# Performance work log

Measured on AMD Instinct MI355X. Metric: run time of the kernel, lower is better.

## Reference

```python
import jax, jax.numpy as jnp
import numpy as np

MAX_DIM = 1024
VOCAB = 257
DEPTH = 6
Q_DIM = MAX_DIM // 4  # 256
EXP_DIMS = [1, 2, 4, 8, 16, 32, 64, 128]  # expander sizes: current_q doubles up to Q_DIM
BATCH, SEQ = 8, 4096


def qlinear(q, W):
    """Quaternion Hamilton-product linear.
    q: [..., in, 4] (last dim = r,i,j,k components), W: [4, out, in] (stacked r,i,j,k weights).
    Returns [..., out, 4].
    """
    # P[..., o, w, a] = F.linear(component_a, W_w)  -> all 16 small GEMMs in one einsum
    P = jnp.einsum('...ia,woi->...owa', q, W)
    Pr, Pi, Pj, Pk = P[..., 0, :], P[..., 1, :], P[..., 2, :], P[..., 3, :]  # each [..., out, 4]
    out_r = Pr[..., 0] - Pi[..., 1] - Pj[..., 2] - Pk[..., 3]
    out_i = Pi[..., 0] + Pr[..., 1] + Pk[..., 2] - Pj[..., 3]
    out_j = Pj[..., 0] - Pk[..., 1] + Pr[..., 2] + Pi[..., 3]
    out_k = Pk[..., 0] + Pj[..., 1] - Pi[..., 2] + Pr[..., 3]
    return jnp.stack([out_r, out_i, out_j, out_k], axis=-1)


def qnormalize(q):
    norm = jnp.linalg.norm(q, axis=-1, keepdims=True)
    return q / (norm + 1e-8)


def setup_inputs() -> dict:
    key = jax.random.key(0)
    ks = jax.random.split(key, 4 + len(EXP_DIMS))
    inp = {}
    inp['x'] = jax.random.randint(ks[0], (BATCH, SEQ), 0, VOCAB)
    inp['emb'] = jax.random.normal(ks[1], (VOCAB, 4), dtype=jnp.float32)
    for idx, cq in enumerate(EXP_DIMS):
        scale = cq ** (-0.5)
        inp[f'w_exp{idx}'] = jax.random.uniform(ks[2 + idx], (4, cq, cq), jnp.float32, -scale, scale)
    scale = Q_DIM ** (-0.5)
    inp['w_layers'] = jax.random.uniform(ks[-2], (DEPTH, 4, Q_DIM, Q_DIM), jnp.float32, -scale, scale)
    inp['w_head'] = jax.random.normal(ks[-1], (VOCAB, MAX_DIM), dtype=jnp.float32) * MAX_DIM ** (-0.5)
    return inp


def reference(x, emb, w_exp0, w_exp1, w_exp2, w_exp3, w_exp4, w_exp5, w_exp6, w_exp7,
              w_layers, w_head):
    q = emb[x][:, :, None, :]  # [B, S, 1, 4]
    for w in (w_exp0, w_exp1, w_exp2, w_exp3, w_exp4, w_exp5, w_exp6, w_exp7):
        delta = jnp.tanh(qlinear(q, w))
        q = jnp.concatenate([q + delta, q - delta], axis=2)  # doubles quaternion dim
    for d in range(DEPTH):
        q = qnormalize(qlinear(q, w_layers[d]))
    stability_loss = jnp.mean(jnp.abs(q[..., 0]))
    h_flat = q.reshape(x.shape[0], x.shape[1], -1)  # [B, S, MAX_DIM]
    logits = jnp.einsum('bsd,vd->bsv', h_flat, w_head)
    return (logits, stability_loss)
```

## Files before the change

kernel.cpp:

```cpp
#include <hip/hip_runtime.h>


typedef _Float16 f16x8 __attribute__((ext_vector_type(8)));
typedef float    f32x4 __attribute__((ext_vector_type(4)));

#define GL2LDS16(gp, lp) __builtin_amdgcn_global_load_lds(                     \
    (const __attribute__((address_space(1))) void*)(gp),                       \
    (__attribute__((address_space(3))) void*)(lp), 16, 0, 0)

__device__ __forceinline__ unsigned short f2h(float f) {
  union { _Float16 h; unsigned short u; } c;
  c.h = (_Float16)f;
  return c.u;
}
__device__ __forceinline__ float h2f(unsigned short u) {
  union { unsigned short u; _Float16 h; } c;
  c.u = u;
  return (float)c.h;
}

__global__ __launch_bounds__(256) void expand_ham(
    const float* __restrict__ w, unsigned short* __restrict__ out,
    int cq, int kbits, int total) {
  int id = blockIdx.x * 256 + threadIdx.x;
  if (id >= total) return;
  const int K = 1 << kbits;
  const int n = id >> kbits;
  const int k = id & (K - 1);
  float val = 0.f;
  if (n < 4 * cq) {
    const int o = n >> 2, a = n & 3, i = k >> 2, b = k & 3;
    const int   comp[4][4] = {{0,1,2,3},{1,0,3,2},{2,3,0,1},{3,2,1,0}};
    const float sgn [4][4] = {{1.f,-1.f,-1.f,-1.f},{1.f,1.f,1.f,-1.f},
                              {1.f,-1.f,1.f,1.f},{1.f,1.f,-1.f,1.f}};
    val = sgn[a][b] * w[comp[a][b] * cq * cq + o * cq + i];
  }
  out[id] = f2h(val);
}

__global__ __launch_bounds__(256) void expand_ham6(
    const float* __restrict__ w, unsigned short* __restrict__ out) {
  const int id = blockIdx.x * 256 + threadIdx.x;
  const int d = id >> 20;
  const int r = id & 1048575;
  const int n = r >> 10, k = r & 1023;
  const int o = n >> 2, a = n & 3, i = k >> 2, b = k & 3;
  const int   comp[4][4] = {{0,1,2,3},{1,0,3,2},{2,3,0,1},{3,2,1,0}};
  const float sgn [4][4] = {{1.f,-1.f,-1.f,-1.f},{1.f,1.f,1.f,-1.f},
                            {1.f,-1.f,1.f,1.f},{1.f,1.f,-1.f,1.f}};
  const float val =
      sgn[a][b] * w[d * 262144 + comp[a][b] * 65536 + o * 256 + i];
  out[id] = f2h(val);
}

__global__ __launch_bounds__(256) void conv_head(
    const float* __restrict__ wh, unsigned short* __restrict__ out) {
  int id = blockIdx.x * 256 + threadIdx.x;
  int v = id >> 10, k = id & 1023;
  out[id] = f2h(v < 257 ? wh[v * 1024 + k] : 0.f);
}

template <int CQ>
__device__ __forceinline__ void exp_step(float (&q)[16][4],
                                         const float* __restrict__ w) {
  float d[CQ][4];
#pragma unroll
  for (int o = 0; o < CQ; o++) {
    float pr = 0.f, pi = 0.f, pj = 0.f, pk = 0.f;
#pragma unroll
    for (int i = 0; i < CQ; i++) {
      const float wr = w[0 * CQ * CQ + o * CQ + i];
      const float wi = w[1 * CQ * CQ + o * CQ + i];
      const float wj = w[2 * CQ * CQ + o * CQ + i];
      const float wk = w[3 * CQ * CQ + o * CQ + i];
      const float qr = q[i][0], qi = q[i][1], qj = q[i][2], qk = q[i][3];
      pr += wr * qr - wi * qi - wj * qj - wk * qk;
      pi += wi * qr + wr * qi + wk * qj - wj * qk;
      pj += wj * qr - wk * qi + wr * qj + wi * qk;
      pk += wk * qr + wj * qi - wi * qj + wr * qk;
    }
    d[o][0] = tanhf(pr); d[o][1] = tanhf(pi);
    d[o][2] = tanhf(pj); d[o][3] = tanhf(pk);
  }
#pragma unroll
  for (int o = 0; o < CQ; o++)
#pragma unroll
    for (int a = 0; a < 4; a++) {
      const float dd = d[o][a], qq = q[o][a];
      q[o][a]      = qq + dd;
      q[CQ + o][a] = qq - dd;
    }
}

__global__ __launch_bounds__(256) void embed_expand(
    const int* __restrict__ x, const float* __restrict__ emb,
    const float* __restrict__ w0, const float* __restrict__ w1,
    const float* __restrict__ w2, const float* __restrict__ w3,
    unsigned short* __restrict__ out) {
  const int t = blockIdx.x * 256 + threadIdx.x;
  float q[16][4];
  const int v = x[t];
  const float4 e = *(const float4*)(emb + v * 4);
  q[0][0] = e.x; q[0][1] = e.y; q[0][2] = e.z; q[0][3] = e.w;
  exp_step<1>(q, w0);
  exp_step<2>(q, w1);
  exp_step<4>(q, w2);
  exp_step<8>(q, w3);
  ushort4* o4 = (ushort4*)(out + (size_t)t * 64);
#pragma unroll
  for (int c = 0; c < 16; c++) {
    ushort4 u;
    u.x = f2h(q[c][0]); u.y = f2h(q[c][1]);
    u.z = f2h(q[c][2]); u.w = f2h(q[c][3]);
    o4[c] = u;
  }
}

template <int EPI>
__global__ __launch_bounds__(256) void gemm_epi(
    const unsigned short* __restrict__ W,
    const unsigned short* __restrict__ Act,
    unsigned short* __restrict__ OutB, float* __restrict__ OutF,
    int K, int Nreal, int ldout) {
  __shared__ unsigned short WtL[128 * 32];
  __shared__ unsigned short WtH[128 * 32];
  __shared__ unsigned short AtL[128 * 32];
  __shared__ unsigned short AtH[128 * 32];

  const int tid  = threadIdx.x;
  const int wave = tid >> 6;
  const int lane = tid & 63;
  const int l15  = lane & 15;
  const int quad = lane >> 4;

  const int Gx = gridDim.x;
  const int L  = blockIdx.y * Gx + blockIdx.x;
  const int j  = L & 7;
  const int s  = L >> 3;
  const int nblock = (s % Gx) * 128;
  const int mblock = (32 * j + s / Gx) * 128;
  const int wn = (wave & 1) * 64;
  const int wm = (wave >> 1) * 64;

  f32x4 acc[4][4];
  const f32x4 zero = {0.f, 0.f, 0.f, 0.f};
#pragma unroll
  for (int a = 0; a < 4; a++)
#pragma unroll
    for (int b = 0; b < 4; b++) acc[a][b] = zero;

  const int row0 = tid >> 2;
  const int sub  = tid & 3;
  const unsigned short* gW0 = W   + (size_t)(nblock + row0)      * K + sub * 8;
  const unsigned short* gW1 = W   + (size_t)(nblock + row0 + 64) * K + sub * 8;
  const unsigned short* gA0 = Act + (size_t)(mblock + row0)      * K + sub * 8;
  const unsigned short* gA1 = Act + (size_t)(mblock + row0 + 64) * K + sub * 8;
  unsigned short* lWL0 = &WtL[wave * 512];
  unsigned short* lWL1 = &WtL[2048 + wave * 512];
  unsigned short* lWH0 = &WtH[wave * 512];
  unsigned short* lWH1 = &WtH[2048 + wave * 512];
  unsigned short* lAL0 = &AtL[wave * 512];
  unsigned short* lAL1 = &AtL[2048 + wave * 512];
  unsigned short* lAH0 = &AtH[wave * 512];
  unsigned short* lAH1 = &AtH[2048 + wave * 512];

  for (int kb = 0; kb < K; kb += 64) {
    GL2LDS16(gW0 + kb,      lWL0);
    GL2LDS16(gW1 + kb,      lWL1);
    GL2LDS16(gW0 + kb + 32, lWH0);
    GL2LDS16(gW1 + kb + 32, lWH1);
    GL2LDS16(gA0 + kb,      lAL0);
    GL2LDS16(gA1 + kb,      lAL1);
    GL2LDS16(gA0 + kb + 32, lAH0);
    GL2LDS16(gA1 + kb + 32, lAH1);
    __syncthreads();

    {
      f16x8 afr[4], bfr[4];
#pragma unroll
      for (int tn = 0; tn < 4; tn++)
        afr[tn] = *(const f16x8*)&WtL[(wn + tn * 16 + l15) * 32 + quad * 8];
#pragma unroll
      for (int tm = 0; tm < 4; tm++)
        bfr[tm] = *(const f16x8*)&AtL[(wm + tm * 16 + l15) * 32 + quad * 8];
#pragma unroll
      for (int tn = 0; tn < 4; tn++)
#pragma unroll
        for (int tm = 0; tm < 4; tm++)
          acc[tn][tm] = __builtin_amdgcn_mfma_f32_16x16x32_f16(
              afr[tn], bfr[tm], acc[tn][tm], 0, 0, 0);
    }
    {
      f16x8 afr[4], bfr[4];
#pragma unroll
      for (int tn = 0; tn < 4; tn++)
        afr[tn] = *(const f16x8*)&WtH[(wn + tn * 16 + l15) * 32 + quad * 8];
#pragma unroll
      for (int tm = 0; tm < 4; tm++)
        bfr[tm] = *(const f16x8*)&AtH[(wm + tm * 16 + l15) * 32 + quad * 8];
#pragma unroll
      for (int tn = 0; tn < 4; tn++)
#pragma unroll
        for (int tm = 0; tm < 4; tm++)
          acc[tn][tm] = __builtin_amdgcn_mfma_f32_16x16x32_f16(
              afr[tn], bfr[tm], acc[tn][tm], 0, 0, 0);
    }
    __syncthreads();
  }

#pragma unroll
  for (int tn = 0; tn < 4; tn++) {
    const int n = nblock + wn + tn * 16 + quad * 4;
    if (n < Nreal) {
#pragma unroll
      for (int tm = 0; tm < 4; tm++) {
        const int token = mblock + wm + tm * 16 + l15;
        const f32x4 v = acc[tn][tm];
        const unsigned short* ip = Act + (size_t)token * K + n;
        const float i0 = h2f(ip[0]), i1 = h2f(ip[1]);
        const float i2 = h2f(ip[2]), i3 = h2f(ip[3]);
        const float d0 = tanhf(v[0]), d1 = tanhf(v[1]);
        const float d2 = tanhf(v[2]), d3 = tanhf(v[3]);
        ushort4 up, um;
        up.x = f2h(i0 + d0); up.y = f2h(i1 + d1);
        up.z = f2h(i2 + d2); up.w = f2h(i3 + d3);
        um.x = f2h(i0 - d0); um.y = f2h(i1 - d1);
        um.z = f2h(i2 - d2); um.w = f2h(i3 - d3);
        *(ushort4*)&OutB[(size_t)token * ldout + n] = up;
        *(ushort4*)&OutB[(size_t)token * ldout + Nreal + n] = um;
      }
    }
  }
}

template <int EPI>
__global__ __launch_bounds__(256, 4) void gemm8p(
    const unsigned short* __restrict__ W,
    const unsigned short* __restrict__ Act,
    unsigned short* __restrict__ OutB, float* __restrict__ OutF,
    int K, int NW, int ldout) {
  __shared__ unsigned short S[2 * 8192];
  __shared__ float lsum[4];

  const int tid  = threadIdx.x;
  const int wave = tid >> 6;
  const int lane = tid & 63;
  const int l15  = lane & 15;
  const int quad = lane >> 4;
  const int wr   = wave >> 1;
  const int wc   = wave & 1;

  const int Gx = gridDim.x;
  const int L  = blockIdx.y * Gx + blockIdx.x;
  const int j  = L & 7;
  const int s  = L >> 3;
  const int mblock = (j * (gridDim.y >> 3) + s / Gx) * 128;
  const int nblock = (s % Gx) * 128;
  const int NT = K >> 5;

  f32x4 acc[4][4];
  const f32x4 zero = {0.f, 0.f, 0.f, 0.f};
#pragma unroll
  for (int a = 0; a < 4; a++)
#pragma unroll
    for (int b = 0; b < 4; b++) acc[a][b] = zero;

  const int rw = tid >> 2;
  const int sl = (tid & 3) ^ ((tid >> 3) & 3);
  const int wrow0 = nblock + rw;
  const int wrow1 = nblock + 64 + rw;
  const int cw0 = wrow0 < NW ? wrow0 : NW - 1;
  const int cw1 = wrow1 < NW ? wrow1 : NW - 1;
  const unsigned short* sW0 = W   + (size_t)cw0 * K + sl * 8;
  const unsigned short* sW1 = W   + (size_t)cw1 * K + sl * 8;
  const unsigned short* sB0 = Act + (size_t)(mblock + rw)      * K + sl * 8;
  const unsigned short* sB1 = Act + (size_t)(mblock + 64 + rw) * K + sl * 8;

  const int swz = (quad * 8) ^ ((l15 & 6) << 2);

  {
    unsigned short* d0 = S + tid * 8;
    GL2LDS16(sW0, d0);
    GL2LDS16(sW1, d0 + 2048);
    GL2LDS16(sB0, d0 + 4096);
    GL2LDS16(sB1, d0 + 6144);
    if (NT > 1) {
      unsigned short* d1 = S + 8192 + tid * 8;
      GL2LDS16(sW0 + 32, d1);
      GL2LDS16(sW1 + 32, d1 + 2048);
      GL2LDS16(sB0 + 32, d1 + 4096);
      GL2LDS16(sB1 + 32, d1 + 6144);
      asm volatile("s_waitcnt vmcnt(4)" ::: "memory");
    } else {
      asm volatile("s_waitcnt vmcnt(0)" ::: "memory");
    }
  }
  __builtin_amdgcn_s_barrier();
  __builtin_amdgcn_sched_barrier(0);

#pragma unroll 2
  for (int kt = 0; kt < NT; ++kt) {
    const unsigned short* SA = S + (kt & 1) * 8192;
    const unsigned short* SB = SA + 4096;

    f16x8 af[4], bf[4];
#pragma unroll
    for (int t4 = 0; t4 < 4; t4++)
      af[t4] = *(const f16x8*)(SA + (wr * 64 + t4 * 16 + l15) * 32 + swz);
#pragma unroll
    for (int t4 = 0; t4 < 4; t4++)
      bf[t4] = *(const f16x8*)(SB + (wc * 64 + t4 * 16 + l15) * 32 + swz);

    asm volatile("s_waitcnt lgkmcnt(0)" ::: "memory");
    __builtin_amdgcn_s_barrier();
    __builtin_amdgcn_sched_barrier(0);
    if (kt + 2 < NT) {
      const int kb = (kt + 2) * 32;
      unsigned short* d = S + (kt & 1) * 8192 + tid * 8;
      GL2LDS16(sW0 + kb, d);
      GL2LDS16(sW1 + kb, d + 2048);
      GL2LDS16(sB0 + kb, d + 4096);
      GL2LDS16(sB1 + kb, d + 6144);
    }

    __builtin_amdgcn_s_setprio(1);
#pragma unroll
    for (int tn = 0; tn < 4; tn++)
#pragma unroll
      for (int tm = 0; tm < 4; tm++)
        acc[tn][tm] = __builtin_amdgcn_mfma_f32_16x16x32_f16(
            af[tn], bf[tm], acc[tn][tm], 0, 0, 0);
    __builtin_amdgcn_s_setprio(0);

    if (kt < NT - 1) {
      if (kt + 2 < NT) asm volatile("s_waitcnt vmcnt(4)" ::: "memory");
      else             asm volatile("s_waitcnt vmcnt(0)" ::: "memory");
      __builtin_amdgcn_s_barrier();
      __builtin_amdgcn_sched_barrier(0);
    }
  }

  if constexpr (EPI == 0) {
#pragma unroll
    for (int tn = 0; tn < 4; tn++) {
      const int n = nblock + wr * 64 + tn * 16 + quad * 4;
#pragma unroll
      for (int tm = 0; tm < 4; tm++) {
        const int token = mblock + wc * 64 + tm * 16 + l15;
        const f32x4 v = acc[tn][tm];
        const unsigned short* ip = Act + (size_t)token * K + n;
        const float i0 = h2f(ip[0]), i1 = h2f(ip[1]);
        const float i2 = h2f(ip[2]), i3 = h2f(ip[3]);
        const float d0 = tanhf(v[0]), d1 = tanhf(v[1]);
        const float d2 = tanhf(v[2]), d3 = tanhf(v[3]);
        ushort4 up, um;
        up.x = f2h(i0 + d0); up.y = f2h(i1 + d1);
        up.z = f2h(i2 + d2); up.w = f2h(i3 + d3);
        um.x = f2h(i0 - d0); um.y = f2h(i1 - d1);
        um.z = f2h(i2 - d2); um.w = f2h(i3 - d3);
        *(ushort4*)&OutB[(size_t)token * ldout + n] = up;
        *(ushort4*)&OutB[(size_t)token * ldout + NW + n] = um;
      }
    }
  } else if constexpr (EPI == 1 || EPI == 2) {
    float loss = 0.f;
#pragma unroll
    for (int tn = 0; tn < 4; tn++) {
      const int n = nblock + wr * 64 + tn * 16 + quad * 4;
#pragma unroll
      for (int tm = 0; tm < 4; tm++) {
        const int token = mblock + wc * 64 + tm * 16 + l15;
        const f32x4 v = acc[tn][tm];
        const float nrm =
            sqrtf(v[0] * v[0] + v[1] * v[1] + v[2] * v[2] + v[3] * v[3]);
        const float inv = 1.f / (nrm + 1e-8f);
        ushort4 u;
        u.x = f2h(v[0] * inv); u.y = f2h(v[1] * inv);
        u.z = f2h(v[2] * inv); u.w = f2h(v[3] * inv);
        *(ushort4*)&OutB[(size_t)token * 1024 + n] = u;
        if constexpr (EPI == 2) loss += fabsf(v[0] * inv);
      }
    }
    if constexpr (EPI == 2) {
#pragma unroll
      for (int off = 32; off > 0; off >>= 1) loss += __shfl_down(loss, off);
      if (lane == 0) lsum[wave] = loss;
      __syncthreads();
      if (tid == 0) {
        float t = lsum[0] + lsum[1] + lsum[2] + lsum[3];
        atomicAdd(OutF, t * (1.f / 8388608.f));
      }
    }
  } else {
#pragma unroll
    for (int tn = 0; tn < 4; tn++) {
      const int n = nblock + wr * 64 + tn * 16 + quad * 4;
      if (n < 257) {
#pragma unroll
        for (int tm = 0; tm < 4; tm++) {
          const int token = mblock + wc * 64 + tm * 16 + l15;
          const f32x4 v = acc[tn][tm];
#pragma unroll
          for (int r = 0; r < 4; r++)
            if (n + r < 257) OutF[(size_t)token * 257 + n + r] = v[r];
        }
      }
    }
  }
}

extern "C" void kernel_launch(void* const* d_in, const int* in_sizes, int n_in,
                              void* d_out, int out_size, void* d_ws,
                              size_t ws_size, hipStream_t stream) {
  const int*   x    = (const int*)d_in[0];
  const float* emb  = (const float*)d_in[1];
  const float* we0  = (const float*)d_in[2];
  const float* we1  = (const float*)d_in[3];
  const float* we2  = (const float*)d_in[4];
  const float* we3  = (const float*)d_in[5];
  const float* we4  = (const float*)d_in[6];
  const float* we5  = (const float*)d_in[7];
  const float* we6  = (const float*)d_in[8];
  const float* we7  = (const float*)d_in[9];
  const float* wlay = (const float*)d_in[10];
  const float* wh   = (const float*)d_in[11];
  float* out = (float*)d_out;

  char* p = (char*)d_ws;
  auto alloc = [&](size_t bytes) {
    void* r = (void*)p;
    p += (bytes + 255) & ~(size_t)255;
    return r;
  };
  unsigned short* act0 = (unsigned short*)alloc(32768ull * 1024 * 2);
  unsigned short* act1 = (unsigned short*)alloc(32768ull * 1024 * 2);
  unsigned short* E4 = (unsigned short*)alloc(128 * 64 * 2);
  unsigned short* E5 = (unsigned short*)alloc(128 * 128 * 2);
  unsigned short* E6 = (unsigned short*)alloc(256 * 256 * 2);
  unsigned short* E7 = (unsigned short*)alloc(512 * 512 * 2);
  unsigned short* EL = (unsigned short*)alloc(6ull * 1024 * 1024 * 2);
  unsigned short* WH = (unsigned short*)alloc(384 * 1024 * 2);

  hipMemsetAsync(out + 8421376, 0, 4, stream);

  expand_ham<<<dim3(8192 / 256), 256, 0, stream>>>(we4, E4, 16, 6, 128 * 64);
  expand_ham<<<dim3(16384 / 256), 256, 0, stream>>>(we5, E5, 32, 7, 128 * 128);
  expand_ham<<<dim3(65536 / 256), 256, 0, stream>>>(we6, E6, 64, 8, 256 * 256);
  expand_ham<<<dim3(262144 / 256), 256, 0, stream>>>(we7, E7, 128, 9,
                                                     512 * 512);
  expand_ham6<<<dim3(6 * 1048576 / 256), 256, 0, stream>>>(wlay, EL);
  conv_head<<<dim3(384 * 1024 / 256), 256, 0, stream>>>(wh, WH);

  embed_expand<<<dim3(128), 256, 0, stream>>>(x, emb, we0, we1, we2, we3, act0);

  gemm_epi<0><<<dim3(1, 256), 256, 0, stream>>>(E4, act0, act1, nullptr, 64,
                                                64, 128);
  gemm_epi<0><<<dim3(1, 256), 256, 0, stream>>>(E5, act1, act0, nullptr, 128,
                                                128, 256);
  gemm8p<0><<<dim3(2, 256), 256, 0, stream>>>(E6, act0, act1, nullptr, 256,
                                              256, 512);
  gemm8p<0><<<dim3(4, 256), 256, 0, stream>>>(E7, act1, act0, nullptr, 512,
                                              512, 1024);

  unsigned short* a = act0;
  unsigned short* b = act1;
  for (int d = 0; d < 5; d++) {
    gemm8p<1><<<dim3(8, 256), 256, 0, stream>>>(EL + (size_t)d * 1048576, a, b,
                                                nullptr, 1024, 1024, 1024);
    unsigned short* t = a; a = b; b = t;
  }
  gemm8p<2><<<dim3(8, 256), 256, 0, stream>>>(EL + 5ull * 1048576, a, b,
                                              out + 8421376, 1024, 1024, 1024);
  { unsigned short* t = a; a = b; b = t; }

  gemm8p<3><<<dim3(3, 256), 256, 0, stream>>>(WH, a, nullptr, out, 1024, 384,
                                              0);
}
```

Before: 973.9 us.

## Load activation operand directly into registers and retile GEMM to 64x256 blocks

Replaces the 128x128 LDS-staged GEMM with a 64(N)x256(M) tile. Each wave loads its own 64 activation rows straight from global memory into registers with inline-asm dwordx4 loads, and only the weight tile is staged through LDS in a 4-deep ring buffer. This cuts LDS traffic and LDS reads for the activation operand and shrinks shared memory per block. The costs are higher register pressure (launch bounds drop to 3 blocks per CU), uncoalesced row-strided global loads, and no W row clamping for the head GEMM. The head weights are padded to 384 rows, so that case stays in bounds.

```diff
diff --git a/kernel.cpp b/kernel.cpp
--- a/kernel.cpp
+++ b/kernel.cpp
@@ -7,6 +7,10 @@
 #define GL2LDS16(gp, lp) __builtin_amdgcn_global_load_lds(                     \
     (const __attribute__((address_space(1))) void*)(gp),                       \
     (__attribute__((address_space(3))) void*)(lp), 16, 0, 0)
+
+#define BLOAD(dst, voff, imm)                                                  \
+  asm volatile("global_load_dwordx4 %0, %1, %2 offset:" #imm                   \
+               : "=v"(dst) : "v"(voff), "s"(bbase))
 
 __device__ __forceinline__ unsigned short f2h(float f) {
   union { _Float16 h; unsigned short u; } c;
@@ -234,12 +238,12 @@
 }
 
 template <int EPI>
-__global__ __launch_bounds__(256, 4) void gemm8p(
+__global__ __launch_bounds__(256, 3) void gemm_bg(
     const unsigned short* __restrict__ W,
     const unsigned short* __restrict__ Act,
     unsigned short* __restrict__ OutB, float* __restrict__ OutF,
     int K, int NW, int ldout) {
-  __shared__ unsigned short S[2 * 8192];
+  __shared__ unsigned short S[4 * 2048];
   __shared__ float lsum[4];
 
   const int tid  = threadIdx.x;
@@ -247,15 +251,13 @@
   const int lane = tid & 63;
   const int l15  = lane & 15;
   const int quad = lane >> 4;
-  const int wr   = wave >> 1;
-  const int wc   = wave & 1;
 
   const int Gx = gridDim.x;
   const int L  = blockIdx.y * Gx + blockIdx.x;
   const int j  = L & 7;
   const int s  = L >> 3;
-  const int mblock = (j * (gridDim.y >> 3) + s / Gx) * 128;
-  const int nblock = (s % Gx) * 128;
+  const int mblock = (j * (gridDim.y >> 3) + s / Gx) * 256;
+  const int nblock = (s % Gx) * 64;
   const int NT = K >> 5;
 
   f32x4 acc[4][4];
@@ -265,88 +267,117 @@
 #pragma unroll
     for (int b = 0; b < 4; b++) acc[a][b] = zero;
 
-  const int rw = tid >> 2;
   const int sl = (tid & 3) ^ ((tid >> 3) & 3);
-  const int wrow0 = nblock + rw;
-  const int wrow1 = nblock + 64 + rw;
-  const int cw0 = wrow0 < NW ? wrow0 : NW - 1;
-  const int cw1 = wrow1 < NW ? wrow1 : NW - 1;
-  const unsigned short* sW0 = W   + (size_t)cw0 * K + sl * 8;
-  const unsigned short* sW1 = W   + (size_t)cw1 * K + sl * 8;
-  const unsigned short* sB0 = Act + (size_t)(mblock + rw)      * K + sl * 8;
-  const unsigned short* sB1 = Act + (size_t)(mblock + 64 + rw) * K + sl * 8;
+  const unsigned short* sW = W + (size_t)(nblock + (tid >> 2)) * K + sl * 8;
 
   const int swz = (quad * 8) ^ ((l15 & 6) << 2);
 
-  {
-    unsigned short* d0 = S + tid * 8;
-    GL2LDS16(sW0, d0);
-    GL2LDS16(sW1, d0 + 2048);
-    GL2LDS16(sB0, d0 + 4096);
-    GL2LDS16(sB1, d0 + 6144);
-    if (NT > 1) {
-      unsigned short* d1 = S + 8192 + tid * 8;
-      GL2LDS16(sW0 + 32, d1);
-      GL2LDS16(sW1 + 32, d1 + 2048);
-      GL2LDS16(sB0 + 32, d1 + 4096);
-      GL2LDS16(sB1 + 32, d1 + 6144);
-      asm volatile("s_waitcnt vmcnt(4)" ::: "memory");
-    } else {
-      asm volatile("s_waitcnt vmcnt(0)" ::: "memory");
-    }
-  }
+  const unsigned long long bbase =
+      (unsigned long long)(const unsigned short*)(Act + (size_t)mblock * K);
+  unsigned int vb0 = (unsigned)(((wave * 64 +  0 + l15) * K + quad * 8) * 2);
+  unsigned int vb1 = (unsigned)(((wave * 64 + 16 + l15) * K + quad * 8) * 2);
+  unsigned int vb2 = (unsigned)(((wave * 64 + 32 + l15) * K + quad * 8) * 2);
+  unsigned int vb3 = (unsigned)(((wave * 64 + 48 + l15) * K + quad * 8) * 2);
+
+  f16x8 ba0, ba1, ba2, ba3, bb0, bb1, bb2, bb3;
+
+  BLOAD(ba0, vb0, 0); BLOAD(ba1, vb1, 0);
+  BLOAD(ba2, vb2, 0); BLOAD(ba3, vb3, 0);
+  __builtin_amdgcn_sched_barrier(0);
+  GL2LDS16(sW, S + tid * 8);
+  __builtin_amdgcn_sched_barrier(0);
+  GL2LDS16(sW + 32, S + 2048 + tid * 8);
+  __builtin_amdgcn_sched_barrier(0);
+  BLOAD(bb0, vb0, 64); BLOAD(bb1, vb1, 64);
+  BLOAD(bb2, vb2, 64); BLOAD(bb3, vb3, 64);
+  vb0 += 128; vb1 += 128; vb2 += 128; vb3 += 128;
+  asm volatile("s_waitcnt vmcnt(5)" ::: "memory");
   __builtin_amdgcn_s_barrier();
   __builtin_amdgcn_sched_barrier(0);
 
-#pragma unroll 2
-  for (int kt = 0; kt < NT; ++kt) {
-    const unsigned short* SA = S + (kt & 1) * 8192;
-    const unsigned short* SB = SA + 4096;
-
-    f16x8 af[4], bf[4];
-#pragma unroll
-    for (int t4 = 0; t4 < 4; t4++)
-      af[t4] = *(const f16x8*)(SA + (wr * 64 + t4 * 16 + l15) * 32 + swz);
-#pragma unroll
-    for (int t4 = 0; t4 < 4; t4++)
-      bf[t4] = *(const f16x8*)(SB + (wc * 64 + t4 * 16 + l15) * 32 + swz);
-
-    asm volatile("s_waitcnt lgkmcnt(0)" ::: "memory");
-    __builtin_amdgcn_s_barrier();
-    __builtin_amdgcn_sched_barrier(0);
-    if (kt + 2 < NT) {
-      const int kb = (kt + 2) * 32;
-      unsigned short* d = S + (kt & 1) * 8192 + tid * 8;
-      GL2LDS16(sW0 + kb, d);
-      GL2LDS16(sW1 + kb, d + 2048);
-      GL2LDS16(sB0 + kb, d + 4096);
-      GL2LDS16(sB1 + kb, d + 6144);
-    }
-
-    __builtin_amdgcn_s_setprio(1);
-#pragma unroll
-    for (int tn = 0; tn < 4; tn++)
-#pragma unroll
-      for (int tm = 0; tm < 4; tm++)
-        acc[tn][tm] = __builtin_amdgcn_mfma_f32_16x16x32_f16(
-            af[tn], bf[tm], acc[tn][tm], 0, 0, 0);
-    __builtin_amdgcn_s_setprio(0);
-
-    if (kt < NT - 1) {
-      if (kt + 2 < NT) asm volatile("s_waitcnt vmcnt(4)" ::: "memory");
-      else             asm volatile("s_waitcnt vmcnt(0)" ::: "memory");
+  for (int kt = 0; kt < NT; kt += 2) {
+    {
+      const unsigned short* Ab = S + ((kt & 3) << 11);
+      const f16x8 af0 = *(const f16x8*)(Ab + ( 0 + l15) * 32 + swz);
+      const f16x8 af1 = *(const f16x8*)(Ab + (16 + l15) * 32 + swz);
+      const f16x8 af2 = *(const f16x8*)(Ab + (32 + l15) * 32 + swz);
+      const f16x8 af3 = *(const f16x8*)(Ab + (48 + l15) * 32 + swz);
+      __builtin_amdgcn_s_setprio(1);
+      acc[0][0] = __builtin_amdgcn_mfma_f32_16x16x32_f16(af0, ba0, acc[0][0], 0, 0, 0);
+      acc[0][1] = __builtin_amdgcn_mfma_f32_16x16x32_f16(af0, ba1, acc[0][1], 0, 0, 0);
+      acc[0][2] = __builtin_amdgcn_mfma_f32_16x16x32_f16(af0, ba2, acc[0][2], 0, 0, 0);
+      acc[0][3] = __builtin_amdgcn_mfma_f32_16x16x32_f16(af0, ba3, acc[0][3], 0, 0, 0);
+      acc[1][0] = __builtin_amdgcn_mfma_f32_16x16x32_f16(af1, ba0, acc[1][0], 0, 0, 0);
+      acc[1][1] = __builtin_amdgcn_mfma_f32_16x16x32_f16(af1, ba1, acc[1][1], 0, 0, 0);
+      acc[1][2] = __builtin_amdgcn_mfma_f32_16x16x32_f16(af1, ba2, acc[1][2], 0, 0, 0);
+      acc[1][3] = __builtin_amdgcn_mfma_f32_16x16x32_f16(af1, ba3, acc[1][3], 0, 0, 0);
+      acc[2][0] = __builtin_amdgcn_mfma_f32_16x16x32_f16(af2, ba0, acc[2][0], 0, 0, 0);
+      acc[2][1] = __builtin_amdgcn_mfma_f32_16x16x32_f16(af2, ba1, acc[2][1], 0, 0, 0);
+      acc[2][2] = __builtin_amdgcn_mfma_f32_16x16x32_f16(af2, ba2, acc[2][2], 0, 0, 0);
+      acc[2][3] = __builtin_amdgcn_mfma_f32_16x16x32_f16(af2, ba3, acc[2][3], 0, 0, 0);
+      acc[3][0] = __builtin_amdgcn_mfma_f32_16x16x32_f16(af3, ba0, acc[3][0], 0, 0, 0);
+      acc[3][1] = __builtin_amdgcn_mfma_f32_16x16x32_f16(af3, ba1, acc[3][1], 0, 0, 0);
+      acc[3][2] = __builtin_amdgcn_mfma_f32_16x16x32_f16(af3, ba2, acc[3][2], 0, 0, 0);
+      acc[3][3] = __builtin_amdgcn_mfma_f32_16x16x32_f16(af3, ba3, acc[3][3], 0, 0, 0);
+      __builtin_amdgcn_s_setprio(0);
+      if (kt + 2 < NT) {
+        BLOAD(ba0, vb0, 0); BLOAD(ba1, vb1, 0);
+        BLOAD(ba2, vb2, 0); BLOAD(ba3, vb3, 0);
+        GL2LDS16(sW + (kt + 2) * 32, S + (((kt + 2) & 3) << 11) + tid * 8);
+        asm volatile("s_waitcnt vmcnt(5)" ::: "memory");
+      } else {
+        asm volatile("s_waitcnt vmcnt(0)" ::: "memory");
+      }
       __builtin_amdgcn_s_barrier();
       __builtin_amdgcn_sched_barrier(0);
     }
+    {
+      const unsigned short* Ab = S + (((kt + 1) & 3) << 11);
+      const f16x8 af0 = *(const f16x8*)(Ab + ( 0 + l15) * 32 + swz);
+      const f16x8 af1 = *(const f16x8*)(Ab + (16 + l15) * 32 + swz);
+      const f16x8 af2 = *(const f16x8*)(Ab + (32 + l15) * 32 + swz);
+      const f16x8 af3 = *(const f16x8*)(Ab + (48 + l15) * 32 + swz);
+      __builtin_amdgcn_s_setprio(1);
+      acc[0][0] = __builtin_amdgcn_mfma_f32_16x16x32_f16(af0, bb0, acc[0][0], 0, 0, 0);
+      acc[0][1] = __builtin_amdgcn_mfma_f32_16x16x32_f16(af0, bb1, acc[0][1], 0, 0, 0);
+      acc[0][2] = __builtin_amdgcn_mfma_f32_16x16x32_f16(af0, bb2, acc[0][2], 0, 0, 0);
+      acc[0][3] = __builtin_amdgcn_mfma_f32_16x16x32_f16(af0, bb3, acc[0][3], 0, 0, 0);
+      acc[1][0] = __builtin_amdgcn_mfma_f32_16x16x32_f16(af1, bb0, acc[1][0], 0, 0, 0);
+      acc[1][1] = __builtin_amdgcn_mfma_f32_16x16x32_f16(af1, bb1, acc[1][1], 0, 0, 0);
+      acc[1][2] = __builtin_amdgcn_mfma_f32_16x16x32_f16(af1, bb2, acc[1][2], 0, 0, 0);
+      acc[1][3] = __builtin_amdgcn_mfma_f32_16x16x32_f16(af1, bb3, acc[1][3], 0, 0, 0);
+      acc[2][0] = __builtin_amdgcn_mfma_f32_16x16x32_f16(af2, bb0, acc[2][0], 0, 0, 0);
+      acc[2][1] = __builtin_amdgcn_mfma_f32_16x16x32_f16(af2, bb1, acc[2][1], 0, 0, 0);
+      acc[2][2] = __builtin_amdgcn_mfma_f32_16x16x32_f16(af2, bb2, acc[2][2], 0, 0, 0);
+      acc[2][3] = __builtin_amdgcn_mfma_f32_16x16x32_f16(af2, bb3, acc[2][3], 0, 0, 0);
+      acc[3][0] = __builtin_amdgcn_mfma_f32_16x16x32_f16(af3, bb0, acc[3][0], 0, 0, 0);
+      acc[3][1] = __builtin_amdgcn_mfma_f32_16x16x32_f16(af3, bb1, acc[3][1], 0, 0, 0);
+      acc[3][2] = __builtin_amdgcn_mfma_f32_16x16x32_f16(af3, bb2, acc[3][2], 0, 0, 0);
+      acc[3][3] = __builtin_amdgcn_mfma_f32_16x16x32_f16(af3, bb3, acc[3][3], 0, 0, 0);
+      __builtin_amdgcn_s_setprio(0);
+      const bool pf2 = (kt + 3) < NT;
+      if (pf2) {
+        BLOAD(bb0, vb0, 64); BLOAD(bb1, vb1, 64);
+        BLOAD(bb2, vb2, 64); BLOAD(bb3, vb3, 64);
+        GL2LDS16(sW + (kt + 3) * 32, S + (((kt + 3) & 3) << 11) + tid * 8);
+      }
+      vb0 += 128; vb1 += 128; vb2 += 128; vb3 += 128;
+      if (kt + 1 < NT - 1) {
+        if (pf2) asm volatile("s_waitcnt vmcnt(5)" ::: "memory");
+        else     asm volatile("s_waitcnt vmcnt(0)" ::: "memory");
+        __builtin_amdgcn_s_barrier();
+        __builtin_amdgcn_sched_barrier(0);
+      }
+    }
   }
 
   if constexpr (EPI == 0) {
 #pragma unroll
     for (int tn = 0; tn < 4; tn++) {
-      const int n = nblock + wr * 64 + tn * 16 + quad * 4;
+      const int n = nblock + tn * 16 + quad * 4;
 #pragma unroll
       for (int tm = 0; tm < 4; tm++) {
-        const int token = mblock + wc * 64 + tm * 16 + l15;
+        const int token = mblock + wave * 64 + tm * 16 + l15;
         const f32x4 v = acc[tn][tm];
         const unsigned short* ip = Act + (size_t)token * K + n;
         const float i0 = h2f(ip[0]), i1 = h2f(ip[1]);
@@ -366,10 +397,10 @@
     float loss = 0.f;
 #pragma unroll
     for (int tn = 0; tn < 4; tn++) {
-      const int n = nblock + wr * 64 + tn * 16 + quad * 4;
+      const int n = nblock + tn * 16 + quad * 4;
 #pragma unroll
       for (int tm = 0; tm < 4; tm++) {
-        const int token = mblock + wc * 64 + tm * 16 + l15;
+        const int token = mblock + wave * 64 + tm * 16 + l15;
         const f32x4 v = acc[tn][tm];
         const float nrm =
             sqrtf(v[0] * v[0] + v[1] * v[1] + v[2] * v[2] + v[3] * v[3]);
@@ -394,11 +425,11 @@
   } else {
 #pragma unroll
     for (int tn = 0; tn < 4; tn++) {
-      const int n = nblock + wr * 64 + tn * 16 + quad * 4;
+      const int n = nblock + tn * 16 + quad * 4;
       if (n < 257) {
 #pragma unroll
         for (int tm = 0; tm < 4; tm++) {
-          const int token = mblock + wc * 64 + tm * 16 + l15;
+          const int token = mblock + wave * 64 + tm * 16 + l15;
           const f32x4 v = acc[tn][tm];
 #pragma unroll
           for (int r = 0; r < 4; r++)
@@ -457,22 +488,23 @@
                                                 64, 128);
   gemm_epi<0><<<dim3(1, 256), 256, 0, stream>>>(E5, act1, act0, nullptr, 128,
                                                 128, 256);
-  gemm8p<0><<<dim3(2, 256), 256, 0, stream>>>(E6, act0, act1, nullptr, 256,
-                                              256, 512);
-  gemm8p<0><<<dim3(4, 256), 256, 0, stream>>>(E7, act1, act0, nullptr, 512,
-                                              512, 1024);
+  gemm_bg<0><<<dim3(4, 128), 256, 0, stream>>>(E6, act0, act1, nullptr, 256,
+                                               256, 512);
+  gemm_bg<0><<<dim3(8, 128), 256, 0, stream>>>(E7, act1, act0, nullptr, 512,
+                                               512, 1024);
 
   unsigned short* a = act0;
   unsigned short* b = act1;
   for (int d = 0; d < 5; d++) {
-    gemm8p<1><<<dim3(8, 256), 256, 0, stream>>>(EL + (size_t)d * 1048576, a, b,
-                                                nullptr, 1024, 1024, 1024);
+    gemm_bg<1><<<dim3(16, 128), 256, 0, stream>>>(EL + (size_t)d * 1048576, a,
+                                                  b, nullptr, 1024, 1024, 1024);
     unsigned short* t = a; a = b; b = t;
   }
-  gemm8p<2><<<dim3(8, 256), 256, 0, stream>>>(EL + 5ull * 1048576, a, b,
-                                              out + 8421376, 1024, 1024, 1024);
+  gemm_bg<2><<<dim3(16, 128), 256, 0, stream>>>(EL + 5ull * 1048576, a, b,
+                                                out + 8421376, 1024, 1024,
+                                                1024);
   { unsigned short* t = a; a = b; b = t; }
 
-  gemm8p<3><<<dim3(3, 256), 256, 0, stream>>>(WH, a, nullptr, out, 1024, 384,
-                                              0);
-}
+  gemm_bg<3><<<dim3(6, 128), 256, 0, stream>>>(WH, a, nullptr, out, 1024, 384,
+                                               0);
+}
```

Measured after the change: 1.127 ms. 1.16x slower.

## Replace 128x128 GEMM with 256x256 8-wave ping-pong pipelined kernel

Applied to the files above, without the earlier changes.

Rewrites the main fp16 MFMA GEMM from 128x128 tiles with 4 waves and a 32-wide K double buffer to 256x256 tiles with 8 waves and 64-wide K stages held in 128KB of LDS. Global-to-LDS loads are staggered across eight MFMA phases with fine-grained barriers. The aim is more data reuse per tile and better overlap of loads with MFMA work. In exchange it uses much more LDS and registers (a 32-tile accumulator), and the larger tiles leave fewer blocks for the smaller expander and head GEMMs.

```diff
diff --git a/kernel.cpp b/kernel.cpp
--- a/kernel.cpp
+++ b/kernel.cpp
@@ -7,6 +7,15 @@
 #define GL2LDS16(gp, lp) __builtin_amdgcn_global_load_lds(                     \
     (const __attribute__((address_space(1))) void*)(gp),                       \
     (__attribute__((address_space(3))) void*)(lp), 16, 0, 0)
+
+#define STG(slot, isB, half, PT, kb)                                           \
+  do {                                                                         \
+    GL2LDS16(PT[half][0] + (kb),                                               \
+             S + (slot) * 32768 + (isB) * 16384 + (half) * 8192 + tid * 8);    \
+    GL2LDS16(PT[half][1] + (kb),                                               \
+             S + (slot) * 32768 + (isB) * 16384 + (half) * 8192 + 4096 +       \
+                 tid * 8);                                                     \
+  } while (0)
 
 __device__ __forceinline__ unsigned short f2h(float f) {
   union { _Float16 h; unsigned short u; } c;
@@ -234,116 +243,134 @@
 }
 
 template <int EPI>
-__global__ __launch_bounds__(256, 4) void gemm8p(
+__global__ __launch_bounds__(512, 2) void gemm_8ph(
     const unsigned short* __restrict__ W,
     const unsigned short* __restrict__ Act,
     unsigned short* __restrict__ OutB, float* __restrict__ OutF,
     int K, int NW, int ldout) {
-  __shared__ unsigned short S[2 * 8192];
-  __shared__ float lsum[4];
+  __shared__ unsigned short S[65536];
+  __shared__ float lsum[8];
 
   const int tid  = threadIdx.x;
   const int wave = tid >> 6;
   const int lane = tid & 63;
   const int l15  = lane & 15;
   const int quad = lane >> 4;
-  const int wr   = wave >> 1;
-  const int wc   = wave & 1;
+  const int wr   = wave >> 2;
+  const int wc   = wave & 3;
 
   const int Gx = gridDim.x;
   const int L  = blockIdx.y * Gx + blockIdx.x;
   const int j  = L & 7;
   const int s  = L >> 3;
-  const int mblock = (j * (gridDim.y >> 3) + s / Gx) * 128;
-  const int nblock = (s % Gx) * 128;
-  const int NT = K >> 5;
-
-  f32x4 acc[4][4];
+  const int mblock = (j * (gridDim.y >> 3) + s / Gx) * 256;
+  const int nblock = (s % Gx) * 256;
+  const int NI = K >> 7;
+
+  f32x4 acc[8][4];
   const f32x4 zero = {0.f, 0.f, 0.f, 0.f};
 #pragma unroll
-  for (int a = 0; a < 4; a++)
+  for (int a = 0; a < 8; a++)
 #pragma unroll
     for (int b = 0; b < 4; b++) acc[a][b] = zero;
 
-  const int rw = tid >> 2;
-  const int sl = (tid & 3) ^ ((tid >> 3) & 3);
-  const int wrow0 = nblock + rw;
-  const int wrow1 = nblock + 64 + rw;
-  const int cw0 = wrow0 < NW ? wrow0 : NW - 1;
-  const int cw1 = wrow1 < NW ? wrow1 : NW - 1;
-  const unsigned short* sW0 = W   + (size_t)cw0 * K + sl * 8;
-  const unsigned short* sW1 = W   + (size_t)cw1 * K + sl * 8;
-  const unsigned short* sB0 = Act + (size_t)(mblock + rw)      * K + sl * 8;
-  const unsigned short* sB1 = Act + (size_t)(mblock + 64 + rw) * K + sl * 8;
-
-  const int swz = (quad * 8) ^ ((l15 & 6) << 2);
-
-  {
-    unsigned short* d0 = S + tid * 8;
-    GL2LDS16(sW0, d0);
-    GL2LDS16(sW1, d0 + 2048);
-    GL2LDS16(sB0, d0 + 4096);
-    GL2LDS16(sB1, d0 + 6144);
-    if (NT > 1) {
-      unsigned short* d1 = S + 8192 + tid * 8;
-      GL2LDS16(sW0 + 32, d1);
-      GL2LDS16(sW1 + 32, d1 + 2048);
-      GL2LDS16(sB0 + 32, d1 + 4096);
-      GL2LDS16(sB1 + 32, d1 + 6144);
-      asm volatile("s_waitcnt vmcnt(4)" ::: "memory");
-    } else {
-      asm volatile("s_waitcnt vmcnt(0)" ::: "memory");
-    }
-  }
+  const int r8 = tid >> 3;
+  const int s8 = (tid & 7) ^ (r8 & 7);
+  const unsigned short* pW[2][2];
+  const unsigned short* pB[2][2];
+#pragma unroll
+  for (int h = 0; h < 2; h++)
+#pragma unroll
+    for (int g = 0; g < 2; g++) {
+      int wrow = nblock + h * 128 + g * 64 + r8;
+      if (wrow >= NW) wrow = NW - 1;
+      pW[h][g] = W   + (size_t)wrow * K + s8 * 8;
+      pB[h][g] = Act + (size_t)(mblock + h * 128 + g * 64 + r8) * K + s8 * 8;
+    }
+
+  const int lrow = l15 * 64;
+  const int ksw0 = ((quad)     ^ (l15 & 7)) * 8;
+  const int ksw1 = ((4 + quad) ^ (l15 & 7)) * 8;
+
+  STG(0, 0, 0, pW, 0);  STG(0, 0, 1, pW, 0);
+  STG(0, 1, 0, pB, 0);  STG(0, 1, 1, pB, 0);
+  STG(1, 1, 0, pB, 64); STG(1, 1, 1, pB, 64);
+  asm volatile("s_waitcnt vmcnt(4)" ::: "memory");
   __builtin_amdgcn_s_barrier();
   __builtin_amdgcn_sched_barrier(0);
 
-#pragma unroll 2
-  for (int kt = 0; kt < NT; ++kt) {
-    const unsigned short* SA = S + (kt & 1) * 8192;
-    const unsigned short* SB = SA + 4096;
-
-    f16x8 af[4], bf[4];
-#pragma unroll
-    for (int t4 = 0; t4 < 4; t4++)
-      af[t4] = *(const f16x8*)(SA + (wr * 64 + t4 * 16 + l15) * 32 + swz);
-#pragma unroll
-    for (int t4 = 0; t4 < 4; t4++)
-      bf[t4] = *(const f16x8*)(SB + (wc * 64 + t4 * 16 + l15) * 32 + swz);
-
-    asm volatile("s_waitcnt lgkmcnt(0)" ::: "memory");
-    __builtin_amdgcn_s_barrier();
-    __builtin_amdgcn_sched_barrier(0);
-    if (kt + 2 < NT) {
-      const int kb = (kt + 2) * 32;
-      unsigned short* d = S + (kt & 1) * 8192 + tid * 8;
-      GL2LDS16(sW0 + kb, d);
-      GL2LDS16(sW1 + kb, d + 2048);
-      GL2LDS16(sB0 + kb, d + 4096);
-      GL2LDS16(sB1 + kb, d + 6144);
-    }
-
-    __builtin_amdgcn_s_setprio(1);
-#pragma unroll
-    for (int tn = 0; tn < 4; tn++)
-#pragma unroll
-      for (int tm = 0; tm < 4; tm++)
-        acc[tn][tm] = __builtin_amdgcn_mfma_f32_16x16x32_f16(
-            af[tn], bf[tm], acc[tn][tm], 0, 0, 0);
-    __builtin_amdgcn_s_setprio(0);
-
-    if (kt < NT - 1) {
-      if (kt + 2 < NT) asm volatile("s_waitcnt vmcnt(4)" ::: "memory");
-      else             asm volatile("s_waitcnt vmcnt(0)" ::: "memory");
+  f16x8 bfr[4][2];
+  for (int i = 0; i < NI; ++i) {
+    const bool nl = (i < NI - 1);
+    const int kA1 = (2 * i + 1) * 64;
+    const int k2  = (2 * i + 2) * 64;
+    const int k3  = (2 * i + 3) * 64;
+#pragma unroll
+    for (int p = 0; p < 8; ++p) {
+      const int q  = p & 3;
+      const int sb = (p >> 2) * 32768;
+      if (q == 0) {
+#pragma unroll
+        for (int c = 0; c < 4; ++c) {
+          const unsigned short* bp = S + sb + 16384 + (wc * 64 + c * 16) * 64
+                                       + lrow;
+          bfr[c][0] = *(const f16x8*)(bp + ksw0);
+          bfr[c][1] = *(const f16x8*)(bp + ksw1);
+        }
+      }
+      f16x8 af[2][2];
+#pragma unroll
+      for (int f = 0; f < 2; ++f) {
+        const unsigned short* ap = S + sb + (wr * 128 + q * 32 + f * 16) * 64
+                                     + lrow;
+        af[f][0] = *(const f16x8*)(ap + ksw0);
+        af[f][1] = *(const f16x8*)(ap + ksw1);
+      }
+      if      (p == 0) { STG(1, 0, 0, pW, kA1); }
+      else if (p == 1) { STG(1, 0, 1, pW, kA1); }
+      else if (p == 2) { if (nl) STG(0, 1, 0, pB, k2); }
+      else if (p == 3) { if (nl) STG(0, 1, 1, pB, k2); }
+      else if (p == 4) { if (nl) STG(0, 0, 0, pW, k2); }
+      else if (p == 5) { if (nl) STG(0, 0, 1, pW, k2); }
+      else if (p == 6) { if (nl) STG(1, 1, 0, pB, k3); }
+      else             { if (nl) STG(1, 1, 1, pB, k3); }
+
       __builtin_amdgcn_s_barrier();
+      asm volatile("s_waitcnt lgkmcnt(0)" ::: "memory");
       __builtin_amdgcn_sched_barrier(0);
+      __builtin_amdgcn_s_setprio(1);
+#pragma unroll
+      for (int f = 0; f < 2; ++f)
+#pragma unroll
+        for (int c = 0; c < 4; ++c) {
+          acc[q * 2 + f][c] = __builtin_amdgcn_mfma_f32_16x16x32_f16(
+              af[f][0], bfr[c][0], acc[q * 2 + f][c], 0, 0, 0);
+          acc[q * 2 + f][c] = __builtin_amdgcn_mfma_f32_16x16x32_f16(
+              af[f][1], bfr[c][1], acc[q * 2 + f][c], 0, 0, 0);
+        }
+      __builtin_amdgcn_s_setprio(0);
+
+      if (p == 3) {
+        if (nl) asm volatile("s_waitcnt vmcnt(4)" ::: "memory");
+        else    asm volatile("s_waitcnt vmcnt(0)" ::: "memory");
+        __builtin_amdgcn_s_barrier();
+        __builtin_amdgcn_sched_barrier(0);
+      } else if (p == 7) {
+        if (nl) {
+          asm volatile("s_waitcnt vmcnt(4)" ::: "memory");
+          __builtin_amdgcn_s_barrier();
+          __builtin_amdgcn_sched_barrier(0);
+        }
+      } else {
+        __builtin_amdgcn_s_barrier();
+      }
     }
   }
 
   if constexpr (EPI == 0) {
 #pragma unroll
-    for (int tn = 0; tn < 4; tn++) {
-      const int n = nblock + wr * 64 + tn * 16 + quad * 4;
+    for (int tn = 0; tn < 8; tn++) {
+      const int n = nblock + wr * 128 + tn * 16 + quad * 4;
 #pragma unroll
       for (int tm = 0; tm < 4; tm++) {
         const int token = mblock + wc * 64 + tm * 16 + l15;
@@ -365,8 +392,8 @@
   } else if constexpr (EPI == 1 || EPI == 2) {
     float loss = 0.f;
 #pragma unroll
-    for (int tn = 0; tn < 4; tn++) {
-      const int n = nblock + wr * 64 + tn * 16 + quad * 4;
+    for (int tn = 0; tn < 8; tn++) {
+      const int n = nblock + wr * 128 + tn * 16 + quad * 4;
 #pragma unroll
       for (int tm = 0; tm < 4; tm++) {
         const int token = mblock + wc * 64 + tm * 16 + l15;
@@ -387,14 +414,16 @@
       if (lane == 0) lsum[wave] = loss;
       __syncthreads();
       if (tid == 0) {
-        float t = lsum[0] + lsum[1] + lsum[2] + lsum[3];
+        float t = 0.f;
+#pragma unroll
+        for (int w8 = 0; w8 < 8; w8++) t += lsum[w8];
         atomicAdd(OutF, t * (1.f / 8388608.f));
       }
     }
   } else {
 #pragma unroll
-    for (int tn = 0; tn < 4; tn++) {
-      const int n = nblock + wr * 64 + tn * 16 + quad * 4;
+    for (int tn = 0; tn < 8; tn++) {
+      const int n = nblock + wr * 128 + tn * 16 + quad * 4;
       if (n < 257) {
 #pragma unroll
         for (int tm = 0; tm < 4; tm++) {
@@ -457,22 +486,23 @@
                                                 64, 128);
   gemm_epi<0><<<dim3(1, 256), 256, 0, stream>>>(E5, act1, act0, nullptr, 128,
                                                 128, 256);
-  gemm8p<0><<<dim3(2, 256), 256, 0, stream>>>(E6, act0, act1, nullptr, 256,
-                                              256, 512);
-  gemm8p<0><<<dim3(4, 256), 256, 0, stream>>>(E7, act1, act0, nullptr, 512,
-                                              512, 1024);
+  gemm_8ph<0><<<dim3(1, 128), 512, 0, stream>>>(E6, act0, act1, nullptr, 256,
+                                                256, 512);
+  gemm_8ph<0><<<dim3(2, 128), 512, 0, stream>>>(E7, act1, act0, nullptr, 512,
+                                                512, 1024);
 
   unsigned short* a = act0;
   unsigned short* b = act1;
   for (int d = 0; d < 5; d++) {
-    gemm8p<1><<<dim3(8, 256), 256, 0, stream>>>(EL + (size_t)d * 1048576, a, b,
-                                                nullptr, 1024, 1024, 1024);
+    gemm_8ph<1><<<dim3(4, 128), 512, 0, stream>>>(EL + (size_t)d * 1048576, a,
+                                                  b, nullptr, 1024, 1024, 1024);
     unsigned short* t = a; a = b; b = t;
   }
-  gemm8p<2><<<dim3(8, 256), 256, 0, stream>>>(EL + 5ull * 1048576, a, b,
-                                              out + 8421376, 1024, 1024, 1024);
+  gemm_8ph<2><<<dim3(4, 128), 512, 0, stream>>>(EL + 5ull * 1048576, a, b,
+                                                out + 8421376, 1024, 1024,
+                                                1024);
   { unsigned short* t = a; a = b; b = t; }
 
-  gemm8p<3><<<dim3(3, 256), 256, 0, stream>>>(WH, a, nullptr, out, 1024, 384,
-                                              0);
-}
+  gemm_8ph<3><<<dim3(2, 128), 512, 0, stream>>>(WH, a, nullptr, out, 1024, 384,
+                                                0);
+}
```

New measurement: 811.4 us. 16.7% less time.
